# Kernel optimization log

Measured on AMD Instinct MI355X. Metric: run time of the kernel, lower is better.

## Reference

```python
import jax, jax.numpy as jnp
import numpy as np

N = 100_000      # nodes
DEG = 16         # avg in-degree (fixed per node for setup)
E = N * DEG      # edges
IN = 256         # in_feats
H = 4            # num_heads
D = 64           # out_feats per head
NEG_SLOPE = 0.2


def setup_inputs() -> dict:
    key = jax.random.key(0)
    k1, k2, k3, k4, k5 = jax.random.split(key, 5)
    # dst-major CSR with uniform degree DEG per destination node
    row_ptr = jnp.arange(N + 1, dtype=jnp.int32) * DEG          # [N+1]
    col_ind = jax.random.randint(k1, (E,), 0, N, dtype=jnp.int32)  # source ids per edge
    feat = jax.random.normal(k2, (N, IN), dtype=jnp.float32)
    # fc.weight (xavier-ish scale), torch Linear: y = x @ W.T
    W = jax.random.normal(k3, (H * D, IN), dtype=jnp.float32) * (1.0 / np.sqrt(IN))
    attn_l = jax.random.normal(k4, (1, H, D), dtype=jnp.float32) * 0.1
    attn_r = jax.random.normal(k5, (1, H, D), dtype=jnp.float32) * 0.1
    return {"row_ptr": row_ptr, "col_ind": col_ind, "feat": feat,
            "W": W, "attn_l": attn_l, "attn_r": attn_r}


def reference(row_ptr, col_ind, feat, W, attn_l, attn_r):
    n_nodes = feat.shape[0]
    n_edges = col_ind.shape[0]
    # feat_src = feat_dst = fc(feat).view(-1, H, D)
    feat_src = (feat @ W.T).reshape(n_nodes, H, D)
    el = jnp.sum(feat_src * attn_l, axis=-1)   # [N, H]
    er = jnp.sum(feat_src * attn_r, axis=-1)   # [N, H]
    # per-edge dst id from CSR row_ptr; src = col_ind
    dst = (jnp.searchsorted(row_ptr, jnp.arange(n_edges, dtype=row_ptr.dtype),
                            side='right') - 1).astype(jnp.int32)
    src = col_ind
    # e = u_add_v(g, er, el) -> er[src] + el[dst], then LeakyReLU
    e = er[src] + el[dst]                      # [E, H]
    e = jnp.where(e > 0, e, NEG_SLOPE * e)
    # CSR edge-softmax: normalize over incoming edges of each dst row
    m = jax.ops.segment_max(e, dst, num_segments=n_nodes)    # [N, H]
    ex = jnp.exp(e - m[dst])
    s = jax.ops.segment_sum(ex, dst, num_segments=n_nodes)   # [N, H]
    a = ex / s[dst]                                          # [E, H]
    # multi-head SpMM: out[n,h] = sum_{e: dst=n} a[e,h] * feat_src[src[e],h]
    outs = []
    for h in range(H):  # small fixed head loop to avoid [E,H,D] intermediate
        msg = a[:, h, None] * feat_src[src, h]               # [E, D]
        outs.append(jax.ops.segment_sum(msg, dst, num_segments=n_nodes))
    return jnp.stack(outs, axis=1)                           # [N, H, D]
```

## Files before the change

### kernel.cpp

```cpp
#include <hip/hip_runtime.h>
#include <math.h>


#define HEADS 4
#define KIN 256
#define NOUT 256
#define NEG_SLOPE 0.2f

typedef __attribute__((ext_vector_type(4))) short short4v;
typedef __attribute__((ext_vector_type(8))) short short8v;
typedef __attribute__((ext_vector_type(4))) float floatx4;

static __device__ __forceinline__ unsigned short f2bf(float x) {
  unsigned u = __float_as_uint(x);
  u += 0x7FFFu + ((u >> 16) & 1u);
  return (unsigned short)(u >> 16);
}
static __device__ __forceinline__ float bf2f(unsigned short b) {
  return __uint_as_float(((unsigned)b) << 16);
}

__global__ __launch_bounds__(256) void k_cast(
    const float* __restrict__ feat, const float* __restrict__ W,
    unsigned short* __restrict__ feat_bf, unsigned short* __restrict__ Wbf,
    int n4) {
  const int stride = gridDim.x * 256;
  for (int i = blockIdx.x * 256 + threadIdx.x; i < n4; i += stride) {
    float4 f = ((const float4*)feat)[i];
    ushort4 o;
    o.x = f2bf(f.x); o.y = f2bf(f.y); o.z = f2bf(f.z); o.w = f2bf(f.w);
    ((ushort4*)feat_bf)[i] = o;
    if (i < (NOUT * KIN / 4)) {
      float4 g = ((const float4*)W)[i];
      ushort4 p;
      p.x = f2bf(g.x); p.y = f2bf(g.y); p.z = f2bf(g.z); p.w = f2bf(g.w);
      ((ushort4*)Wbf)[i] = p;
    }
  }
}

__global__ __launch_bounds__(256, 3) void k_gemm_mfma(
    const unsigned short* __restrict__ feat_bf,
    const unsigned short* __restrict__ Wbf,
    const float* __restrict__ attn_l, const float* __restrict__ attn_r,
    unsigned short* __restrict__ fs_bf, float* __restrict__ el,
    float* __restrict__ er, int n_nodes) {
  __shared__ unsigned short Alds[2][64 * 64];

  const int tid = threadIdx.x;
  const int lane = tid & 63;
  const int w = tid >> 6;
  const int m0 = blockIdx.x * 64;
  const int q = lane >> 4;
  const int l15 = lane & 15;

  floatx4 acc[4][4];
#pragma unroll
  for (int mt = 0; mt < 4; ++mt)
#pragma unroll
    for (int nt = 0; nt < 4; ++nt)
#pragma unroll
      for (int r = 0; r < 4; ++r) acc[mt][nt][r] = 0.0f;

  const int rsub = lane >> 3;
  const int gg = lane & 7;
  const int sg = gg ^ rsub;

  auto stage = [&](int kc, int b) {
#pragma unroll
    for (int s = 0; s < 2; ++s) {
      const int row = w * 16 + s * 8 + rsub;
      int gr = m0 + row;
      if (gr >= n_nodes) gr = n_nodes - 1;
      const unsigned short* src = feat_bf + (size_t)gr * KIN + kc * 64 + sg * 8;
      unsigned short* dst = &Alds[b][(w * 16 + s * 8) * 64];
      __builtin_amdgcn_global_load_lds(
          (const __attribute__((address_space(1))) unsigned int*)src,
          (__attribute__((address_space(3))) unsigned int*)dst, 16, 0, 0);
    }
  };

  stage(0, 0);
  for (int kc = 0; kc < 4; ++kc) {
    __syncthreads();
    if (kc < 3) stage(kc + 1, (kc + 1) & 1);

    short8v bfr[2][4];
#pragma unroll
    for (int ks = 0; ks < 2; ++ks)
#pragma unroll
      for (int nt = 0; nt < 4; ++nt)
        bfr[ks][nt] = *(const short8v*)(Wbf + (size_t)(w * 64 + nt * 16 + l15) * KIN +
                                        kc * 64 + ks * 32 + q * 8);

#pragma unroll
    for (int ks = 0; ks < 2; ++ks) {
      short8v af[4];
#pragma unroll
      for (int mt = 0; mt < 4; ++mt) {
        const int slot = (ks * 4 + q) ^ (l15 & 7);
        af[mt] = *(const short8v*)(&Alds[kc & 1][(mt * 16 + l15) * 64 + slot * 8]);
      }
#pragma unroll
      for (int mt = 0; mt < 4; ++mt)
#pragma unroll
        for (int nt = 0; nt < 4; ++nt)
          acc[mt][nt] = __builtin_amdgcn_mfma_f32_16x16x32_bf16(
              af[mt], bfr[ks][nt], acc[mt][nt], 0, 0, 0);
    }
  }

  float alv[4], arv[4];
#pragma unroll
  for (int nt = 0; nt < 4; ++nt) {
    alv[nt] = attn_l[w * 64 + nt * 16 + l15];
    arv[nt] = attn_r[w * 64 + nt * 16 + l15];
  }
#pragma unroll
  for (int mt = 0; mt < 4; ++mt) {
#pragma unroll
    for (int r = 0; r < 4; ++r) {
      const int m = m0 + mt * 16 + q * 4 + r;
      const bool mvalid = (m < n_nodes);
      float pl = 0.f, pr = 0.f;
#pragma unroll
      for (int nt = 0; nt < 4; ++nt) {
        const float v = acc[mt][nt][r];
        pl = fmaf(v, alv[nt], pl);
        pr = fmaf(v, arv[nt], pr);
        if (mvalid)
          fs_bf[(size_t)m * NOUT + w * 64 + nt * 16 + l15] = f2bf(v);
      }
#pragma unroll
      for (int off = 1; off < 16; off <<= 1) {
        pl += __shfl_xor(pl, off, 64);
        pr += __shfl_xor(pr, off, 64);
      }
      if (l15 == 0 && mvalid) {
        el[m * HEADS + w] = pl;
        er[m * HEADS + w] = pr;
      }
    }
  }
}

__global__ __launch_bounds__(256, 4) void k_aggregate(
    const int* __restrict__ row_ptr, const int* __restrict__ col_ind,
    const float* __restrict__ el, const float* __restrict__ er,
    const unsigned short* __restrict__ fs_bf, float* __restrict__ out,
    int n_nodes) {
  const int gid = blockIdx.x * blockDim.x + threadIdx.x;
  const int node = gid >> 6;
  const int lane = threadIdx.x & 63;
  if (node >= n_nodes) return;

  const int h = lane >> 4;
  const int j = lane & 15;
  const int rs = row_ptr[node];
  const int deg = row_ptr[node + 1] - rs;

  const bool valid = (j < deg);
  const int src = valid ? col_ind[rs + j] : 0;

  float e = valid ? (er[src * HEADS + h] + el[node * HEADS + h]) : -INFINITY;
  e = (e > 0.f) ? e : NEG_SLOPE * e;

  float mx = e;
#pragma unroll
  for (int off = 1; off < 16; off <<= 1) mx = fmaxf(mx, __shfl_xor(mx, off, 64));
  float ex = valid ? __expf(e - mx) : 0.f;
  float s = ex;
#pragma unroll
  for (int off = 1; off < 16; off <<= 1) s += __shfl_xor(s, off, 64);
  const float a = ex / s;

  const int half = lane >> 5;
  const int li = lane & 31;
  const int hd = li >> 3;

  int sj[8];
#pragma unroll
  for (int p = 0; p < 8; ++p) sj[p] = __shfl(src, 2 * p + half, 64);

  uint4 u[8];
#pragma unroll
  for (int p = 0; p < 8; ++p)
    u[p] = ((const uint4*)(fs_bf + (size_t)sj[p] * NOUT))[li];

  float wgt[8];
#pragma unroll
  for (int p = 0; p < 8; ++p)
    wgt[p] = __shfl(a, hd * 16 + 2 * p + half, 64);

  float acc[8];
#pragma unroll
  for (int k = 0; k < 8; ++k) acc[k] = 0.f;
#pragma unroll
  for (int p = 0; p < 8; ++p) {
    const uint4 v = u[p];
    const float w0 = wgt[p];
    acc[0] = fmaf(w0, __uint_as_float(v.x << 16), acc[0]);
    acc[1] = fmaf(w0, __uint_as_float(v.x & 0xFFFF0000u), acc[1]);
    acc[2] = fmaf(w0, __uint_as_float(v.y << 16), acc[2]);
    acc[3] = fmaf(w0, __uint_as_float(v.y & 0xFFFF0000u), acc[3]);
    acc[4] = fmaf(w0, __uint_as_float(v.z << 16), acc[4]);
    acc[5] = fmaf(w0, __uint_as_float(v.z & 0xFFFF0000u), acc[5]);
    acc[6] = fmaf(w0, __uint_as_float(v.w << 16), acc[6]);
    acc[7] = fmaf(w0, __uint_as_float(v.w & 0xFFFF0000u), acc[7]);
  }

#pragma unroll
  for (int k = 0; k < 8; ++k) acc[k] += __shfl_xor(acc[k], 32, 64);

  float4 o;
  o.x = half ? acc[4] : acc[0];
  o.y = half ? acc[5] : acc[1];
  o.z = half ? acc[6] : acc[2];
  o.w = half ? acc[7] : acc[3];
  *(float4*)(out + (size_t)node * NOUT + li * 8 + half * 4) = o;
}

extern "C" void kernel_launch(void* const* d_in, const int* in_sizes, int n_in,
                              void* d_out, int out_size, void* d_ws, size_t ws_size,
                              hipStream_t stream) {
  const int* row_ptr = (const int*)d_in[0];
  const int* col_ind = (const int*)d_in[1];
  const float* feat = (const float*)d_in[2];
  const float* W = (const float*)d_in[3];
  const float* attn_l = (const float*)d_in[4];
  const float* attn_r = (const float*)d_in[5];
  float* out = (float*)d_out;
  const int n_nodes = in_sizes[0] - 1;

  char* ws = (char*)d_ws;
  unsigned short* Wbf = (unsigned short*)ws;
  unsigned short* fs_bf = (unsigned short*)(ws + 128 * 1024);
  size_t fs_bytes = (size_t)n_nodes * NOUT * sizeof(unsigned short);
  float* el = (float*)(ws + 128 * 1024 + fs_bytes);
  float* er = el + (size_t)n_nodes * HEADS;

  unsigned short* feat_bf = (unsigned short*)d_out;

  k_cast<<<2048, 256, 0, stream>>>(feat, W, feat_bf, Wbf, n_nodes * (KIN / 4));
  k_gemm_mfma<<<(n_nodes + 63) / 64, 256, 0, stream>>>(
      feat_bf, Wbf, attn_l, attn_r, fs_bf, el, er, n_nodes);
  k_aggregate<<<(n_nodes + 3) / 4, 256, 0, stream>>>(
      row_ptr, col_ind, el, er, fs_bf, out, n_nodes);
}
```

Measured before the change: 368.3 us.

## Fuse feat fp32-to-bf16 cast into GEMM with register-staged LDS pipeline

Drops the separate full-feature cast kernel. The GEMM now reads fp32 feat directly into registers, converts to bf16 and writes swizzled LDS tiles, prefetching the next K chunk into registers while the current one is computed. This removes a write and re-read of a 51 MB bf16 copy. In exchange it uses more registers (launch bounds lowered to 2 waves/SIMD), does the conversion inside the GEMM, and replaces the async global_load_lds path with a synchronous register round trip.

```diff
diff --git a/kernel.cpp b/kernel.cpp
--- a/kernel.cpp
+++ b/kernel.cpp
@@ -20,28 +20,17 @@
   return __uint_as_float(((unsigned)b) << 16);
 }
 
-__global__ __launch_bounds__(256) void k_cast(
-    const float* __restrict__ feat, const float* __restrict__ W,
-    unsigned short* __restrict__ feat_bf, unsigned short* __restrict__ Wbf,
-    int n4) {
-  const int stride = gridDim.x * 256;
-  for (int i = blockIdx.x * 256 + threadIdx.x; i < n4; i += stride) {
-    float4 f = ((const float4*)feat)[i];
-    ushort4 o;
-    o.x = f2bf(f.x); o.y = f2bf(f.y); o.z = f2bf(f.z); o.w = f2bf(f.w);
-    ((ushort4*)feat_bf)[i] = o;
-    if (i < (NOUT * KIN / 4)) {
-      float4 g = ((const float4*)W)[i];
-      ushort4 p;
-      p.x = f2bf(g.x); p.y = f2bf(g.y); p.z = f2bf(g.z); p.w = f2bf(g.w);
-      ((ushort4*)Wbf)[i] = p;
-    }
-  }
-}
-
-__global__ __launch_bounds__(256, 3) void k_gemm_mfma(
-    const unsigned short* __restrict__ feat_bf,
-    const unsigned short* __restrict__ Wbf,
+__global__ __launch_bounds__(256) void k_cast_w(const float* __restrict__ W,
+                                                unsigned short* __restrict__ Wbf) {
+  const int i = blockIdx.x * 256 + threadIdx.x;
+  float4 f = ((const float4*)W)[i];
+  ushort4 o;
+  o.x = f2bf(f.x); o.y = f2bf(f.y); o.z = f2bf(f.z); o.w = f2bf(f.w);
+  ((ushort4*)Wbf)[i] = o;
+}
+
+__global__ __launch_bounds__(256, 2) void k_gemm_mfma(
+    const float* __restrict__ feat, const unsigned short* __restrict__ Wbf,
     const float* __restrict__ attn_l, const float* __restrict__ attn_r,
     unsigned short* __restrict__ fs_bf, float* __restrict__ el,
     float* __restrict__ er, int n_nodes) {
@@ -62,28 +51,44 @@
 #pragma unroll
       for (int r = 0; r < 4; ++r) acc[mt][nt][r] = 0.0f;
 
-  const int rsub = lane >> 3;
-  const int gg = lane & 7;
-  const int sg = gg ^ rsub;
-
-  auto stage = [&](int kc, int b) {
-#pragma unroll
-    for (int s = 0; s < 2; ++s) {
-      const int row = w * 16 + s * 8 + rsub;
-      int gr = m0 + row;
-      if (gr >= n_nodes) gr = n_nodes - 1;
-      const unsigned short* src = feat_bf + (size_t)gr * KIN + kc * 64 + sg * 8;
-      unsigned short* dst = &Alds[b][(w * 16 + s * 8) * 64];
-      __builtin_amdgcn_global_load_lds(
-          (const __attribute__((address_space(1))) unsigned int*)src,
-          (__attribute__((address_space(3))) unsigned int*)dst, 16, 0, 0);
-    }
-  };
-
-  stage(0, 0);
+  const int ar = tid >> 2;
+  const int aj = tid & 3;
+  const int r7 = ar & 7;
+  int agr = m0 + ar;
+  if (agr >= n_nodes) agr = n_nodes - 1;
+  const float* __restrict__ abase = feat + (size_t)agr * KIN + aj * 16;
+  unsigned short* const aw0 = &Alds[0][ar * 64 + ((2 * aj + 0) ^ r7) * 8];
+  unsigned short* const aw1 = &Alds[0][ar * 64 + ((2 * aj + 1) ^ r7) * 8];
+  const int bufoff = 64 * 64;
+
+  float4 rg[2][4];
+
+#pragma unroll
+  for (int i = 0; i < 4; ++i) rg[0][i] = *(const float4*)(abase + i * 4);
+
+#pragma unroll
   for (int kc = 0; kc < 4; ++kc) {
+    const int b = kc & 1;
+    {
+      const float4* R = rg[b];
+      short8v g0, g1;
+      g0[0] = (short)f2bf(R[0].x); g0[1] = (short)f2bf(R[0].y);
+      g0[2] = (short)f2bf(R[0].z); g0[3] = (short)f2bf(R[0].w);
+      g0[4] = (short)f2bf(R[1].x); g0[5] = (short)f2bf(R[1].y);
+      g0[6] = (short)f2bf(R[1].z); g0[7] = (short)f2bf(R[1].w);
+      g1[0] = (short)f2bf(R[2].x); g1[1] = (short)f2bf(R[2].y);
+      g1[2] = (short)f2bf(R[2].z); g1[3] = (short)f2bf(R[2].w);
+      g1[4] = (short)f2bf(R[3].x); g1[5] = (short)f2bf(R[3].y);
+      g1[6] = (short)f2bf(R[3].z); g1[7] = (short)f2bf(R[3].w);
+      *(short8v*)(aw0 + b * bufoff) = g0;
+      *(short8v*)(aw1 + b * bufoff) = g1;
+    }
+    if (kc < 3) {
+      const float* p = abase + (kc + 1) * 64;
+#pragma unroll
+      for (int i = 0; i < 4; ++i) rg[(kc + 1) & 1][i] = *(const float4*)(p + i * 4);
+    }
     __syncthreads();
-    if (kc < 3) stage(kc + 1, (kc + 1) & 1);
 
     short8v bfr[2][4];
 #pragma unroll
@@ -99,7 +104,7 @@
 #pragma unroll
       for (int mt = 0; mt < 4; ++mt) {
         const int slot = (ks * 4 + q) ^ (l15 & 7);
-        af[mt] = *(const short8v*)(&Alds[kc & 1][(mt * 16 + l15) * 64 + slot * 8]);
+        af[mt] = *(const short8v*)(&Alds[b][(mt * 16 + l15) * 64 + slot * 8]);
       }
 #pragma unroll
       for (int mt = 0; mt < 4; ++mt)
@@ -239,11 +244,9 @@
   float* el = (float*)(ws + 128 * 1024 + fs_bytes);
   float* er = el + (size_t)n_nodes * HEADS;
 
-  unsigned short* feat_bf = (unsigned short*)d_out;
-
-  k_cast<<<2048, 256, 0, stream>>>(feat, W, feat_bf, Wbf, n_nodes * (KIN / 4));
+  k_cast_w<<<64, 256, 0, stream>>>(W, Wbf);
   k_gemm_mfma<<<(n_nodes + 63) / 64, 256, 0, stream>>>(
-      feat_bf, Wbf, attn_l, attn_r, fs_bf, el, er, n_nodes);
+      feat, Wbf, attn_l, attn_r, fs_bf, el, er, n_nodes);
   k_aggregate<<<(n_nodes + 3) / 4, 256, 0, stream>>>(
       row_ptr, col_ind, el, er, fs_bf, out, n_nodes);
 }
```

Result: faster. 349.0 us (-5.2%).
